# Kernel optimization log

Measured on AMD Instinct MI355X. Metric: run time of the kernel, lower is better.

The kernel has to match this reference:

```python
import jax, jax.numpy as jnp
import numpy as np


def setup_inputs() -> dict:
    key = jax.random.key(0)
    ks = jax.random.split(key, 7)
    B, T, D = 4, 4096, 128
    s = 0.02
    return {
        "input_data": jax.random.normal(ks[0], (B, T, D), dtype=jnp.float32),
        "Wq": jax.random.normal(ks[1], (D, D), dtype=jnp.float32) * s,
        "bq": jax.random.normal(ks[2], (D,), dtype=jnp.float32) * s,
        "Wk": jax.random.normal(ks[3], (D, D), dtype=jnp.float32) * s,
        "bk": jax.random.normal(ks[4], (D,), dtype=jnp.float32) * s,
        "Wv": jax.random.normal(ks[5], (D, D), dtype=jnp.float32) * s,
        "bv": jax.random.normal(ks[6], (D,), dtype=jnp.float32) * s,
    }


def reference(input_data, Wq, bq, Wk, bk, Wv, bv):
    D = input_data.shape[-1]
    scale = jnp.asarray(D, input_data.dtype) ** 0.5
    # torch Linear: x @ W.T + b
    q = input_data @ Wq.T + bq  # [B,T,D]
    k = input_data @ Wk.T + bk
    v = input_data @ Wv.T + bv
    energy = jnp.einsum("btd,bsd->bts", q, k) / scale  # [B,T,T]
    attn = jax.nn.softmax(energy, axis=-1)
    return jnp.einsum("bts,bsd->btd", attn, v)  # [B,T,D]
```

## Files before the change

kernel.cpp:

```cpp
#include <hip/hip_runtime.h>
#include <cstdint>

typedef _Float16 half4_t __attribute__((ext_vector_type(4)));
typedef _Float16 half8_t __attribute__((ext_vector_type(8)));
typedef float floatx4 __attribute__((ext_vector_type(4)));

#define T_SEQ 4096
#define D_HEAD 128
#define SCALE_LOG2 0.12751742526f

__device__ __forceinline__ void gload16(const void* src, void* dst_lds) {
    using gptr_t = const __attribute__((address_space(1))) unsigned int*;
    using lptr_t = __attribute__((address_space(3))) unsigned int*;
    __builtin_amdgcn_global_load_lds((gptr_t)(uintptr_t)src,
                                     (lptr_t)(unsigned int)(uintptr_t)dst_lds, 16, 0, 0);
}

__global__ __launch_bounds__(256) void proj_kernel(
    const float* __restrict__ x,
    const float* __restrict__ Wq, const float* __restrict__ bq,
    const float* __restrict__ Wk, const float* __restrict__ bk,
    const float* __restrict__ Wv, const float* __restrict__ bv,
    _Float16* __restrict__ qf, _Float16* __restrict__ kf, _Float16* __restrict__ vt)
{
    __shared__ __align__(16) _Float16 Ws[128 * 136];
    __shared__ __align__(16) _Float16 xs[64 * 136];

    const int t = threadIdx.x;
    const int mat = blockIdx.y;
    const float* W = (mat == 0) ? Wq : (mat == 1) ? Wk : Wv;
    const float* bias = (mat == 0) ? bq : (mat == 1) ? bk : bv;
    const float osc = (mat == 0) ? SCALE_LOG2 : 1.0f;
    const int r0 = blockIdx.x * 64;

    {
        const int o = t >> 1;
        const int i0 = (t & 1) * 64;
        for (int jj = 0; jj < 8; ++jj) {
            floatx4 w0 = *reinterpret_cast<const floatx4*>(W + o * 128 + i0 + jj * 8);
            floatx4 w1 = *reinterpret_cast<const floatx4*>(W + o * 128 + i0 + jj * 8 + 4);
            half8_t h;
            h[0]=(_Float16)w0[0]; h[1]=(_Float16)w0[1]; h[2]=(_Float16)w0[2]; h[3]=(_Float16)w0[3];
            h[4]=(_Float16)w1[0]; h[5]=(_Float16)w1[1]; h[6]=(_Float16)w1[2]; h[7]=(_Float16)w1[3];
            *reinterpret_cast<half8_t*>(&Ws[o * 136 + i0 + jj * 8]) = h;
        }
    }
    {
        const int row = t >> 2;
        const int c0 = (t & 3) * 32;
        for (int jj = 0; jj < 4; ++jj) {
            floatx4 w0 = *reinterpret_cast<const floatx4*>(x + (size_t)(r0 + row) * 128 + c0 + jj * 8);
            floatx4 w1 = *reinterpret_cast<const floatx4*>(x + (size_t)(r0 + row) * 128 + c0 + jj * 8 + 4);
            half8_t h;
            h[0]=(_Float16)w0[0]; h[1]=(_Float16)w0[1]; h[2]=(_Float16)w0[2]; h[3]=(_Float16)w0[3];
            h[4]=(_Float16)w1[0]; h[5]=(_Float16)w1[1]; h[6]=(_Float16)w1[2]; h[7]=(_Float16)w1[3];
            *reinterpret_cast<half8_t*>(&xs[row * 136 + c0 + jj * 8]) = h;
        }
    }
    __syncthreads();

    const int w = t >> 6;
    const int lane = t & 63;
    const int lo = lane & 15, hi = lane >> 4;

    floatx4 acc[8] = {};
    for (int dc = 0; dc < 4; ++dc) {
        half8_t a8 = *reinterpret_cast<const half8_t*>(&xs[(w * 16 + lo) * 136 + dc * 32 + hi * 8]);
        for (int ot = 0; ot < 8; ++ot) {
            half8_t b8 = *reinterpret_cast<const half8_t*>(&Ws[(ot * 16 + lo) * 136 + dc * 32 + hi * 8]);
            acc[ot] = __builtin_amdgcn_mfma_f32_16x16x32_f16(a8, b8, acc[ot], 0, 0, 0);
        }
    }
    __syncthreads();

    float bb[8];
    for (int ot = 0; ot < 8; ++ot) bb[ot] = bias[ot * 16 + lo];

    if (mat < 2) {
        _Float16* ol = xs;
        for (int ot = 0; ot < 8; ++ot)
            for (int r = 0; r < 4; ++r)
                ol[(w * 16 + hi * 4 + r) * 136 + ot * 16 + lo] = (_Float16)((acc[ot][r] + bb[ot]) * osc);
        __syncthreads();
        _Float16* dst = (mat == 0) ? qf : kf;
        for (int i = 0; i < 4; ++i) {
            int c = t + 256 * i;
            int row = c >> 4, p = c & 15;
            half8_t v = *reinterpret_cast<const half8_t*>(&ol[row * 136 + p * 8]);
            *reinterpret_cast<half8_t*>(dst + (size_t)(r0 + row) * 128 + p * 8) = v;
        }
    } else {
        _Float16* vl = Ws;
        for (int ot = 0; ot < 8; ++ot)
            for (int r = 0; r < 4; ++r)
                vl[(ot * 16 + lo) * 72 + w * 16 + hi * 4 + r] = (_Float16)(acc[ot][r] + bb[ot]);
        __syncthreads();
        const int b = r0 >> 12, tl0 = r0 & 4095;
        for (int i = 0; i < 4; ++i) {
            int c = t + 256 * i;
            int d = c >> 3, p = c & 7;
            half8_t v = *reinterpret_cast<const half8_t*>(&vl[d * 72 + p * 8]);
            *reinterpret_cast<half8_t*>(vt + ((size_t)(b * 128 + d)) * 4096 + tl0 + p * 8) = v;
        }
    }
}

__global__ __launch_bounds__(512, 2) void attn_kernel(
    const _Float16* __restrict__ qf, const _Float16* __restrict__ kf,
    const _Float16* __restrict__ vt, float* __restrict__ out)
{
    __shared__ __align__(16) char smem[131072];

    const int tid = threadIdx.x;
    const int w = tid >> 6, lane = tid & 63;
    const int lo = lane & 15, hi = lane >> 4;
    const int qsub = w & 1, split = w >> 1;

    const int bx = blockIdx.x;
    const int wg = (bx & 7) * 32 + (bx >> 3);
    const int b = wg >> 6;
    const int q0 = (wg & 63) * 64;

    const char* kbc = (const char*)(kf + (size_t)b * T_SEQ * 128);
    const char* vbc = (const char*)(vt + (size_t)b * 128 * T_SEQ);

    int koff[4], voff[4], kdst[4], vdst[4];
#pragma unroll
    for (int r = 0; r < 4; ++r) {
        int seg = w * 4 + r;
        int slot = lane & 15;
        int row = seg * 4 + (lane >> 4);
        koff[r] = row * 256 + ((slot ^ (row & 7)) << 4);
        kdst[r] = seg * 1024 + lane * 16;
        int d = row;
        voff[r] = d * (T_SEQ * 2) + ((slot ^ ((d & 7) << 1)) << 4);
        vdst[r] = 32768 + seg * 1024 + lane * 16;
    }

    half8_t qfrag[2][4];
#pragma unroll
    for (int qt = 0; qt < 2; ++qt) {
        const _Float16* qrow = qf + ((size_t)b * T_SEQ + q0 + qsub * 32 + qt * 16 + lo) * 128;
#pragma unroll
        for (int dc = 0; dc < 4; ++dc)
            qfrag[qt][dc] = *reinterpret_cast<const half8_t*>(qrow + dc * 32 + hi * 8);
    }

    floatx4 accO[2][8] = {};
    float m_run[2] = {-1e30f, -1e30f}, l_run[2] = {0.f, 0.f};

#pragma unroll
    for (int r = 0; r < 4; ++r) {
        gload16(kbc + koff[r], smem + kdst[r]);
        gload16(vbc + voff[r], smem + vdst[r]);
    }
    __syncthreads();

    for (int t0 = 0; t0 < T_SEQ; t0 += 128) {
        const int cur = (t0 >> 7) & 1;
        char* buf = smem + (cur << 16);

        if (t0 + 128 < T_SEQ) {
            char* nb = smem + ((cur ^ 1) << 16);
            const char* ks = kbc + (size_t)(t0 + 128) * 256;
            const char* vs = vbc + (size_t)(t0 + 128) * 2;
#pragma unroll
            for (int r = 0; r < 4; ++r) {
                gload16(ks + koff[r], nb + kdst[r]);
                gload16(vs + voff[r], nb + vdst[r]);
            }
        }

        floatx4 sac[2][2] = {};
#pragma unroll
        for (int s = 0; s < 2; ++s) {
            const char* kb0 = buf + (split * 32 + s * 16 + lo) * 256;
            const int rsw = lo & 7;
#pragma unroll
            for (int dc = 0; dc < 4; ++dc) {
                half8_t kf8 = *reinterpret_cast<const half8_t*>(kb0 + (((dc * 4 + hi) ^ rsw) << 4));
                sac[0][s] = __builtin_amdgcn_mfma_f32_16x16x32_f16(kf8, qfrag[0][dc], sac[0][s], 0, 0, 0);
                sac[1][s] = __builtin_amdgcn_mfma_f32_16x16x32_f16(kf8, qfrag[1][dc], sac[1][s], 0, 0, 0);
            }
        }

        float bm[2];
        bool ok = true;
#pragma unroll
        for (int qt = 0; qt < 2; ++qt) {
            float m0 = fmaxf(fmaxf(sac[qt][0][0], sac[qt][0][1]), fmaxf(sac[qt][0][2], sac[qt][0][3]));
            float m1 = fmaxf(fmaxf(sac[qt][1][0], sac[qt][1][1]), fmaxf(sac[qt][1][2], sac[qt][1][3]));
            float m = fmaxf(m0, m1);
            m = fmaxf(m, __shfl_xor(m, 16));
            m = fmaxf(m, __shfl_xor(m, 32));
            bm[qt] = m;
            ok = ok && (m <= m_run[qt] + 4.0f);
        }
        if (!__all(ok)) {
#pragma unroll
            for (int qt = 0; qt < 2; ++qt) {
                float m_new = fmaxf(m_run[qt], bm[qt]);
                float alpha = exp2f(m_run[qt] - m_new);
                l_run[qt] *= alpha;
#pragma unroll
                for (int dt = 0; dt < 8; ++dt) accO[qt][dt] *= alpha;
                m_run[qt] = m_new;
            }
        }
        half8_t pa[2];
#pragma unroll
        for (int qt = 0; qt < 2; ++qt) {
            float bs = 0.f;
            half8_t pp;
#pragma unroll
            for (int s = 0; s < 2; ++s)
#pragma unroll
                for (int r = 0; r < 4; ++r) {
                    float pv = exp2f(sac[qt][s][r] - m_run[qt]);
                    bs += pv;
                    pp[s * 4 + r] = (_Float16)pv;
                }
            bs += __shfl_xor(bs, 16);
            bs += __shfl_xor(bs, 32);
            l_run[qt] += bs;
            pa[qt] = pp;
        }

        const char* vbuf = buf + 32768;
#pragma unroll
        for (int dt = 0; dt < 8; ++dt) {
            int row = dt * 16 + lo;
            const char* vr = vbuf + row * 256;
            int sw = (row & 7) << 1;
            int c0 = split * 4 + (hi >> 1);
            half4_t va = *reinterpret_cast<const half4_t*>(vr + (((c0) ^ sw) << 4) + ((hi & 1) << 3));
            half4_t vb4 = *reinterpret_cast<const half4_t*>(vr + (((c0 + 2) ^ sw) << 4) + ((hi & 1) << 3));
            half8_t vfr;
            vfr[0]=va[0]; vfr[1]=va[1]; vfr[2]=va[2]; vfr[3]=va[3];
            vfr[4]=vb4[0]; vfr[5]=vb4[1]; vfr[6]=vb4[2]; vfr[7]=vb4[3];
            accO[0][dt] = __builtin_amdgcn_mfma_f32_16x16x32_f16(vfr, pa[0], accO[0][dt], 0, 0, 0);
            accO[1][dt] = __builtin_amdgcn_mfma_f32_16x16x32_f16(vfr, pa[1], accO[1][dt], 0, 0, 0);
        }
        __syncthreads();
    }

    float* red_m = reinterpret_cast<float*>(smem + 65536);
    float* red_l = reinterpret_cast<float*>(smem + 65536 + 1024);
    int row64[2]; float fac[2];
#pragma unroll
    for (int qt = 0; qt < 2; ++qt) row64[qt] = qsub * 32 + qt * 16 + lo;
    if (hi == 0) {
#pragma unroll
        for (int qt = 0; qt < 2; ++qt) {
            red_m[split * 64 + row64[qt]] = m_run[qt];
            red_l[split * 64 + row64[qt]] = l_run[qt];
        }
    }
    __syncthreads();
#pragma unroll
    for (int qt = 0; qt < 2; ++qt) {
        float M = -1e30f;
#pragma unroll
        for (int s = 0; s < 4; ++s) M = fmaxf(M, red_m[s * 64 + row64[qt]]);
        float L = 0.f;
#pragma unroll
        for (int s = 0; s < 4; ++s) L += red_l[s * 64 + row64[qt]] * exp2f(red_m[s * 64 + row64[qt]] - M);
        fac[qt] = exp2f(m_run[qt] - M) / L;
    }
    float* out_lds = reinterpret_cast<float*>(smem);
    for (int s = 0; s < 4; ++s) {
        if (split == s) {
#pragma unroll
            for (int qt = 0; qt < 2; ++qt)
#pragma unroll
                for (int dt = 0; dt < 8; ++dt)
#pragma unroll
                    for (int r = 0; r < 4; ++r) {
                        int d = dt * 16 + hi * 4 + r;
                        float v = accO[qt][dt][r] * fac[qt];
                        float* p = &out_lds[row64[qt] * 132 + d];
                        if (s == 0) *p = v; else *p += v;
                    }
        }
        __syncthreads();
    }
    {
        int row = tid >> 3, d0 = (tid & 7) * 16;
        float* op = out + ((size_t)b * T_SEQ + q0 + row) * 128 + d0;
#pragma unroll
        for (int j = 0; j < 4; ++j) {
            float4 v;
            v.x = out_lds[row * 132 + d0 + j * 4 + 0];
            v.y = out_lds[row * 132 + d0 + j * 4 + 1];
            v.z = out_lds[row * 132 + d0 + j * 4 + 2];
            v.w = out_lds[row * 132 + d0 + j * 4 + 3];
            *reinterpret_cast<float4*>(op + j * 4) = v;
        }
    }
}

extern "C" void kernel_launch(void* const* d_in, const int* in_sizes, int n_in,
                              void* d_out, int out_size, void* d_ws, size_t ws_size,
                              hipStream_t stream)
{
    (void)in_sizes; (void)n_in; (void)out_size; (void)ws_size;
    const float* x  = (const float*)d_in[0];
    const float* Wq = (const float*)d_in[1];
    const float* bq = (const float*)d_in[2];
    const float* Wk = (const float*)d_in[3];
    const float* bk = (const float*)d_in[4];
    const float* Wv = (const float*)d_in[5];
    const float* bv = (const float*)d_in[6];
    float* out = (float*)d_out;

    _Float16* qf = (_Float16*)d_ws;
    _Float16* kf = qf + (size_t)4 * T_SEQ * D_HEAD;
    _Float16* vt = kf + (size_t)4 * T_SEQ * D_HEAD;

    proj_kernel<<<dim3(256, 3), 256, 0, stream>>>(x, Wq, bq, Wk, bk, Wv, bv, qf, kf, vt);
    attn_kernel<<<dim3(256), 512, 0, stream>>>(qf, kf, vt, out);
}
```

Baseline: 94.97 us.

## Use 16 waves per attention block, one 16-row query tile per wave

The attention kernel moves from 512 to 1024 threads per block. Each wave now owns a single 16-row query tile instead of two, which halves per-wave accumulators and softmax state and doubles the waves per CU available to hide latency. Each block-wide K/V tile load is split over twice as many threads. The V tile swizzle changes to a plain row-based XOR, with load and read updated to match. s_setprio is raised around the MFMA sections. The cost is that each K and V fragment read from LDS now feeds only one MFMA instead of two, so LDS read traffic per FLOP doubles.

```diff
diff --git a/kernel.cpp b/kernel.cpp
--- a/kernel.cpp
+++ b/kernel.cpp
@@ -105,7 +105,7 @@
     }
 }
 
-__global__ __launch_bounds__(512, 2) void attn_kernel(
+__global__ __launch_bounds__(1024) void attn_kernel(
     const _Float16* __restrict__ qf, const _Float16* __restrict__ kf,
     const _Float16* __restrict__ vt, float* __restrict__ out)
 {
@@ -114,7 +114,7 @@
     const int tid = threadIdx.x;
     const int w = tid >> 6, lane = tid & 63;
     const int lo = lane & 15, hi = lane >> 4;
-    const int qsub = w & 1, split = w >> 1;
+    const int qsub = w & 3, split = w >> 2;
 
     const int bx = blockIdx.x;
     const int wg = (bx & 7) * 32 + (bx >> 3);
@@ -124,33 +124,31 @@
     const char* kbc = (const char*)(kf + (size_t)b * T_SEQ * 128);
     const char* vbc = (const char*)(vt + (size_t)b * 128 * T_SEQ);
 
-    int koff[4], voff[4], kdst[4], vdst[4];
-#pragma unroll
-    for (int r = 0; r < 4; ++r) {
-        int seg = w * 4 + r;
+    int koff[2], voff[2], kdst[2], vdst[2];
+#pragma unroll
+    for (int r = 0; r < 2; ++r) {
+        int seg = w * 2 + r;
         int slot = lane & 15;
         int row = seg * 4 + (lane >> 4);
         koff[r] = row * 256 + ((slot ^ (row & 7)) << 4);
         kdst[r] = seg * 1024 + lane * 16;
-        int d = row;
-        voff[r] = d * (T_SEQ * 2) + ((slot ^ ((d & 7) << 1)) << 4);
+        voff[r] = row * (T_SEQ * 2) + ((slot ^ (row & 7)) << 4);
         vdst[r] = 32768 + seg * 1024 + lane * 16;
     }
 
-    half8_t qfrag[2][4];
-#pragma unroll
-    for (int qt = 0; qt < 2; ++qt) {
-        const _Float16* qrow = qf + ((size_t)b * T_SEQ + q0 + qsub * 32 + qt * 16 + lo) * 128;
+    half8_t qfrag[4];
+    {
+        const _Float16* qrow = qf + ((size_t)b * T_SEQ + q0 + qsub * 16 + lo) * 128;
 #pragma unroll
         for (int dc = 0; dc < 4; ++dc)
-            qfrag[qt][dc] = *reinterpret_cast<const half8_t*>(qrow + dc * 32 + hi * 8);
-    }
-
-    floatx4 accO[2][8] = {};
-    float m_run[2] = {-1e30f, -1e30f}, l_run[2] = {0.f, 0.f};
-
-#pragma unroll
-    for (int r = 0; r < 4; ++r) {
+            qfrag[dc] = *reinterpret_cast<const half8_t*>(qrow + dc * 32 + hi * 8);
+    }
+
+    floatx4 accO[8] = {};
+    float m_run = -1e30f, l_run = 0.f;
+
+#pragma unroll
+    for (int r = 0; r < 2; ++r) {
         gload16(kbc + koff[r], smem + kdst[r]);
         gload16(vbc + voff[r], smem + vdst[r]);
     }
@@ -165,13 +163,14 @@
             const char* ks = kbc + (size_t)(t0 + 128) * 256;
             const char* vs = vbc + (size_t)(t0 + 128) * 2;
 #pragma unroll
-            for (int r = 0; r < 4; ++r) {
+            for (int r = 0; r < 2; ++r) {
                 gload16(ks + koff[r], nb + kdst[r]);
                 gload16(vs + voff[r], nb + vdst[r]);
             }
         }
 
-        floatx4 sac[2][2] = {};
+        floatx4 sac[2] = {};
+        __builtin_amdgcn_s_setprio(1);
 #pragma unroll
         for (int s = 0; s < 2; ++s) {
             const char* kb0 = buf + (split * 32 + s * 16 + lo) * 256;
@@ -179,116 +178,93 @@
 #pragma unroll
             for (int dc = 0; dc < 4; ++dc) {
                 half8_t kf8 = *reinterpret_cast<const half8_t*>(kb0 + (((dc * 4 + hi) ^ rsw) << 4));
-                sac[0][s] = __builtin_amdgcn_mfma_f32_16x16x32_f16(kf8, qfrag[0][dc], sac[0][s], 0, 0, 0);
-                sac[1][s] = __builtin_amdgcn_mfma_f32_16x16x32_f16(kf8, qfrag[1][dc], sac[1][s], 0, 0, 0);
+                sac[s] = __builtin_amdgcn_mfma_f32_16x16x32_f16(kf8, qfrag[dc], sac[s], 0, 0, 0);
             }
         }
-
-        float bm[2];
-        bool ok = true;
-#pragma unroll
-        for (int qt = 0; qt < 2; ++qt) {
-            float m0 = fmaxf(fmaxf(sac[qt][0][0], sac[qt][0][1]), fmaxf(sac[qt][0][2], sac[qt][0][3]));
-            float m1 = fmaxf(fmaxf(sac[qt][1][0], sac[qt][1][1]), fmaxf(sac[qt][1][2], sac[qt][1][3]));
-            float m = fmaxf(m0, m1);
-            m = fmaxf(m, __shfl_xor(m, 16));
-            m = fmaxf(m, __shfl_xor(m, 32));
-            bm[qt] = m;
-            ok = ok && (m <= m_run[qt] + 4.0f);
-        }
+        __builtin_amdgcn_s_setprio(0);
+
+        float m = fmaxf(fmaxf(fmaxf(sac[0][0], sac[0][1]), fmaxf(sac[0][2], sac[0][3])),
+                        fmaxf(fmaxf(sac[1][0], sac[1][1]), fmaxf(sac[1][2], sac[1][3])));
+        m = fmaxf(m, __shfl_xor(m, 16));
+        m = fmaxf(m, __shfl_xor(m, 32));
+        bool ok = (m <= m_run + 4.0f);
         if (!__all(ok)) {
-#pragma unroll
-            for (int qt = 0; qt < 2; ++qt) {
-                float m_new = fmaxf(m_run[qt], bm[qt]);
-                float alpha = exp2f(m_run[qt] - m_new);
-                l_run[qt] *= alpha;
-#pragma unroll
-                for (int dt = 0; dt < 8; ++dt) accO[qt][dt] *= alpha;
-                m_run[qt] = m_new;
+            float m_new = fmaxf(m_run, m);
+            float alpha = exp2f(m_run - m_new);
+            l_run *= alpha;
+#pragma unroll
+            for (int dt = 0; dt < 8; ++dt) accO[dt] *= alpha;
+            m_run = m_new;
+        }
+        half8_t pa;
+        float bs = 0.f;
+#pragma unroll
+        for (int s = 0; s < 2; ++s)
+#pragma unroll
+            for (int r = 0; r < 4; ++r) {
+                float pv = exp2f(sac[s][r] - m_run);
+                bs += pv;
+                pa[s * 4 + r] = (_Float16)pv;
             }
-        }
-        half8_t pa[2];
-#pragma unroll
-        for (int qt = 0; qt < 2; ++qt) {
-            float bs = 0.f;
-            half8_t pp;
-#pragma unroll
-            for (int s = 0; s < 2; ++s)
-#pragma unroll
-                for (int r = 0; r < 4; ++r) {
-                    float pv = exp2f(sac[qt][s][r] - m_run[qt]);
-                    bs += pv;
-                    pp[s * 4 + r] = (_Float16)pv;
-                }
-            bs += __shfl_xor(bs, 16);
-            bs += __shfl_xor(bs, 32);
-            l_run[qt] += bs;
-            pa[qt] = pp;
-        }
+        bs += __shfl_xor(bs, 16);
+        bs += __shfl_xor(bs, 32);
+        l_run += bs;
 
         const char* vbuf = buf + 32768;
+        __builtin_amdgcn_s_setprio(1);
 #pragma unroll
         for (int dt = 0; dt < 8; ++dt) {
             int row = dt * 16 + lo;
             const char* vr = vbuf + row * 256;
-            int sw = (row & 7) << 1;
+            int sw = lo & 7;
             int c0 = split * 4 + (hi >> 1);
-            half4_t va = *reinterpret_cast<const half4_t*>(vr + (((c0) ^ sw) << 4) + ((hi & 1) << 3));
+            half4_t va  = *reinterpret_cast<const half4_t*>(vr + ((c0 ^ sw) << 4) + ((hi & 1) << 3));
             half4_t vb4 = *reinterpret_cast<const half4_t*>(vr + (((c0 + 2) ^ sw) << 4) + ((hi & 1) << 3));
             half8_t vfr;
             vfr[0]=va[0]; vfr[1]=va[1]; vfr[2]=va[2]; vfr[3]=va[3];
             vfr[4]=vb4[0]; vfr[5]=vb4[1]; vfr[6]=vb4[2]; vfr[7]=vb4[3];
-            accO[0][dt] = __builtin_amdgcn_mfma_f32_16x16x32_f16(vfr, pa[0], accO[0][dt], 0, 0, 0);
-            accO[1][dt] = __builtin_amdgcn_mfma_f32_16x16x32_f16(vfr, pa[1], accO[1][dt], 0, 0, 0);
-        }
-        __syncthreads();
-    }
-
-    float* red_m = reinterpret_cast<float*>(smem + 65536);
-    float* red_l = reinterpret_cast<float*>(smem + 65536 + 1024);
-    int row64[2]; float fac[2];
-#pragma unroll
-    for (int qt = 0; qt < 2; ++qt) row64[qt] = qsub * 32 + qt * 16 + lo;
+            accO[dt] = __builtin_amdgcn_mfma_f32_16x16x32_f16(vfr, pa, accO[dt], 0, 0, 0);
+        }
+        __builtin_amdgcn_s_setprio(0);
+        __syncthreads();
+    }
+
+    float* red_m = reinterpret_cast<float*>(smem + 40960);
+    float* red_l = reinterpret_cast<float*>(smem + 43008);
+    const int row16 = qsub * 16 + lo;
     if (hi == 0) {
-#pragma unroll
-        for (int qt = 0; qt < 2; ++qt) {
-            red_m[split * 64 + row64[qt]] = m_run[qt];
-            red_l[split * 64 + row64[qt]] = l_run[qt];
-        }
-    }
-    __syncthreads();
-#pragma unroll
-    for (int qt = 0; qt < 2; ++qt) {
-        float M = -1e30f;
-#pragma unroll
-        for (int s = 0; s < 4; ++s) M = fmaxf(M, red_m[s * 64 + row64[qt]]);
-        float L = 0.f;
-#pragma unroll
-        for (int s = 0; s < 4; ++s) L += red_l[s * 64 + row64[qt]] * exp2f(red_m[s * 64 + row64[qt]] - M);
-        fac[qt] = exp2f(m_run[qt] - M) / L;
-    }
+        red_m[split * 64 + row16] = m_run;
+        red_l[split * 64 + row16] = l_run;
+    }
+    __syncthreads();
+    float M = -1e30f;
+#pragma unroll
+    for (int s = 0; s < 4; ++s) M = fmaxf(M, red_m[s * 64 + row16]);
+    float L = 0.f;
+#pragma unroll
+    for (int s = 0; s < 4; ++s) L += red_l[s * 64 + row16] * exp2f(red_m[s * 64 + row16] - M);
+    const float fac = exp2f(m_run - M) / L;
+
     float* out_lds = reinterpret_cast<float*>(smem);
     for (int s = 0; s < 4; ++s) {
         if (split == s) {
 #pragma unroll
-            for (int qt = 0; qt < 2; ++qt)
-#pragma unroll
-                for (int dt = 0; dt < 8; ++dt)
-#pragma unroll
-                    for (int r = 0; r < 4; ++r) {
-                        int d = dt * 16 + hi * 4 + r;
-                        float v = accO[qt][dt][r] * fac[qt];
-                        float* p = &out_lds[row64[qt] * 132 + d];
-                        if (s == 0) *p = v; else *p += v;
-                    }
-        }
-        __syncthreads();
-    }
-    {
-        int row = tid >> 3, d0 = (tid & 7) * 16;
+            for (int dt = 0; dt < 8; ++dt)
+#pragma unroll
+                for (int r = 0; r < 4; ++r) {
+                    int d = dt * 16 + hi * 4 + r;
+                    float v = accO[dt][r] * fac;
+                    float* p = &out_lds[row16 * 132 + d];
+                    if (s == 0) *p = v; else *p += v;
+                }
+        }
+        __syncthreads();
+    }
+    {
+        int row = tid >> 4, d0 = (tid & 15) * 8;
         float* op = out + ((size_t)b * T_SEQ + q0 + row) * 128 + d0;
 #pragma unroll
-        for (int j = 0; j < 4; ++j) {
+        for (int j = 0; j < 2; ++j) {
             float4 v;
             v.x = out_lds[row * 132 + d0 + j * 4 + 0];
             v.y = out_lds[row * 132 + d0 + j * 4 + 1];
@@ -318,5 +294,5 @@
     _Float16* vt = kf + (size_t)4 * T_SEQ * D_HEAD;
 
     proj_kernel<<<dim3(256, 3), 256, 0, stream>>>(x, Wq, bq, Wk, bk, Wv, bv, qf, kf, vt);
-    attn_kernel<<<dim3(256), 512, 0, stream>>>(qf, kf, vt, out);
-}
+    attn_kernel<<<dim3(256), 1024, 0, stream>>>(qf, kf, vt, out);
+}
```

Result: faster. 92.05 us (-3.1%).

## Stage V tiles through registers with repacked LDS layout, unroll loop, set MFMA priority

Applied to the files above, without the earlier changes.

The V tile prefetch now goes through registers and is written to LDS only after the PV MFMAs. The LDS layout is permuted so each PV operand becomes a single 16-byte read instead of two 8-byte reads plus a shuffle. The main loop is manually unrolled by two with constant buffer offsets and precomputed LDS addresses, s_setprio raises wave priority around the MFMA blocks, and P is converted with packed round-to-zero fp16. Launch bounds drop to one block per CU, which allows more registers per thread at the cost of less occupancy, and the reduction scratch moves to a different LDS offset.

```diff
diff --git a/kernel.cpp b/kernel.cpp
--- a/kernel.cpp
+++ b/kernel.cpp
@@ -1,6 +1,7 @@
 #include <hip/hip_runtime.h>
 #include <cstdint>
 
+typedef _Float16 half2_t __attribute__((ext_vector_type(2)));
 typedef _Float16 half4_t __attribute__((ext_vector_type(4)));
 typedef _Float16 half8_t __attribute__((ext_vector_type(8)));
 typedef float floatx4 __attribute__((ext_vector_type(4)));
@@ -105,7 +106,7 @@
     }
 }
 
-__global__ __launch_bounds__(512, 2) void attn_kernel(
+__global__ __launch_bounds__(512, 1) void attn_kernel(
     const _Float16* __restrict__ qf, const _Float16* __restrict__ kf,
     const _Float16* __restrict__ vt, float* __restrict__ out)
 {
@@ -114,7 +115,7 @@
     const int tid = threadIdx.x;
     const int w = tid >> 6, lane = tid & 63;
     const int lo = lane & 15, hi = lane >> 4;
-    const int qsub = w & 1, split = w >> 1;
+    const int qt2 = w & 1, split = w >> 1;
 
     const int bx = blockIdx.x;
     const int wg = (bx & 7) * 32 + (bx >> 3);
@@ -124,7 +125,7 @@
     const char* kbc = (const char*)(kf + (size_t)b * T_SEQ * 128);
     const char* vbc = (const char*)(vt + (size_t)b * 128 * T_SEQ);
 
-    int koff[4], voff[4], kdst[4], vdst[4];
+    int koff[4], kdst[4];
 #pragma unroll
     for (int r = 0; r < 4; ++r) {
         int seg = w * 4 + r;
@@ -132,15 +133,35 @@
         int row = seg * 4 + (lane >> 4);
         koff[r] = row * 256 + ((slot ^ (row & 7)) << 4);
         kdst[r] = seg * 1024 + lane * 16;
-        int d = row;
-        voff[r] = d * (T_SEQ * 2) + ((slot ^ ((d & 7) << 1)) << 4);
-        vdst[r] = 32768 + seg * 1024 + lane * 16;
-    }
+    }
+
+    const int vc = tid & 15;
+    const int vua = ((vc >> 2) << 2) + ((vc & 1) << 1);
+    const int voffb = (vc & 2) << 2;
+    int vgo[4], vwa[4], vwb[4];
+#pragma unroll
+    for (int i = 0; i < 4; ++i) {
+        int d = (tid >> 4) + 32 * i;
+        vgo[i] = d * (T_SEQ * 2) + vc * 16;
+        vwa[i] = 32768 + d * 256 + (((vua)     ^ (d & 7)) << 4) + voffb;
+        vwb[i] = 32768 + d * 256 + (((vua + 1) ^ (d & 7)) << 4) + voffb;
+    }
+
+    int kro[2][4];
+#pragma unroll
+    for (int s = 0; s < 2; ++s)
+#pragma unroll
+        for (int dc = 0; dc < 4; ++dc)
+            kro[s][dc] = (split * 32 + s * 16 + lo) * 256 + ((((dc * 4 + hi)) ^ (lo & 7)) << 4);
+    int vro[8];
+#pragma unroll
+    for (int dt = 0; dt < 8; ++dt)
+        vro[dt] = 32768 + (dt * 16 + lo) * 256 + (((split * 4 + hi) ^ (lo & 7)) << 4);
 
     half8_t qfrag[2][4];
 #pragma unroll
     for (int qt = 0; qt < 2; ++qt) {
-        const _Float16* qrow = qf + ((size_t)b * T_SEQ + q0 + qsub * 32 + qt * 16 + lo) * 128;
+        const _Float16* qrow = qf + ((size_t)b * T_SEQ + q0 + qt2 * 32 + qt * 16 + lo) * 128;
 #pragma unroll
         for (int dc = 0; dc < 4; ++dc)
             qfrag[qt][dc] = *reinterpret_cast<const half8_t*>(qrow + dc * 32 + hi * 8);
@@ -150,105 +171,117 @@
     float m_run[2] = {-1e30f, -1e30f}, l_run[2] = {0.f, 0.f};
 
 #pragma unroll
-    for (int r = 0; r < 4; ++r) {
-        gload16(kbc + koff[r], smem + kdst[r]);
-        gload16(vbc + voff[r], smem + vdst[r]);
+    for (int r = 0; r < 4; ++r) gload16(kbc + koff[r], smem + kdst[r]);
+    {
+        uint4 vreg[4];
+#pragma unroll
+        for (int i = 0; i < 4; ++i) vreg[i] = *reinterpret_cast<const uint4*>(vbc + vgo[i]);
+#pragma unroll
+        for (int i = 0; i < 4; ++i) {
+            *reinterpret_cast<uint2*>(smem + vwa[i]) = make_uint2(vreg[i].x, vreg[i].y);
+            *reinterpret_cast<uint2*>(smem + vwb[i]) = make_uint2(vreg[i].z, vreg[i].w);
+        }
     }
     __syncthreads();
 
-    for (int t0 = 0; t0 < T_SEQ; t0 += 128) {
-        const int cur = (t0 >> 7) & 1;
-        char* buf = smem + (cur << 16);
-
-        if (t0 + 128 < T_SEQ) {
-            char* nb = smem + ((cur ^ 1) << 16);
-            const char* ks = kbc + (size_t)(t0 + 128) * 256;
-            const char* vs = vbc + (size_t)(t0 + 128) * 2;
-#pragma unroll
-            for (int r = 0; r < 4; ++r) {
-                gload16(ks + koff[r], nb + kdst[r]);
-                gload16(vs + voff[r], nb + vdst[r]);
-            }
-        }
-
-        floatx4 sac[2][2] = {};
-#pragma unroll
-        for (int s = 0; s < 2; ++s) {
-            const char* kb0 = buf + (split * 32 + s * 16 + lo) * 256;
-            const int rsw = lo & 7;
-#pragma unroll
-            for (int dc = 0; dc < 4; ++dc) {
-                half8_t kf8 = *reinterpret_cast<const half8_t*>(kb0 + (((dc * 4 + hi) ^ rsw) << 4));
-                sac[0][s] = __builtin_amdgcn_mfma_f32_16x16x32_f16(kf8, qfrag[0][dc], sac[0][s], 0, 0, 0);
-                sac[1][s] = __builtin_amdgcn_mfma_f32_16x16x32_f16(kf8, qfrag[1][dc], sac[1][s], 0, 0, 0);
-            }
-        }
-
-        float bm[2];
-        bool ok = true;
-#pragma unroll
-        for (int qt = 0; qt < 2; ++qt) {
-            float m0 = fmaxf(fmaxf(sac[qt][0][0], sac[qt][0][1]), fmaxf(sac[qt][0][2], sac[qt][0][3]));
-            float m1 = fmaxf(fmaxf(sac[qt][1][0], sac[qt][1][1]), fmaxf(sac[qt][1][2], sac[qt][1][3]));
-            float m = fmaxf(m0, m1);
-            m = fmaxf(m, __shfl_xor(m, 16));
-            m = fmaxf(m, __shfl_xor(m, 32));
-            bm[qt] = m;
-            ok = ok && (m <= m_run[qt] + 4.0f);
-        }
-        if (!__all(ok)) {
-#pragma unroll
-            for (int qt = 0; qt < 2; ++qt) {
-                float m_new = fmaxf(m_run[qt], bm[qt]);
-                float alpha = exp2f(m_run[qt] - m_new);
-                l_run[qt] *= alpha;
-#pragma unroll
-                for (int dt = 0; dt < 8; ++dt) accO[qt][dt] *= alpha;
-                m_run[qt] = m_new;
-            }
-        }
-        half8_t pa[2];
-#pragma unroll
-        for (int qt = 0; qt < 2; ++qt) {
-            float bs = 0.f;
-            half8_t pp;
-#pragma unroll
-            for (int s = 0; s < 2; ++s)
-#pragma unroll
-                for (int r = 0; r < 4; ++r) {
-                    float pv = exp2f(sac[qt][s][r] - m_run[qt]);
-                    bs += pv;
-                    pp[s * 4 + r] = (_Float16)pv;
-                }
-            bs += __shfl_xor(bs, 16);
-            bs += __shfl_xor(bs, 32);
-            l_run[qt] += bs;
-            pa[qt] = pp;
-        }
-
-        const char* vbuf = buf + 32768;
-#pragma unroll
-        for (int dt = 0; dt < 8; ++dt) {
-            int row = dt * 16 + lo;
-            const char* vr = vbuf + row * 256;
-            int sw = (row & 7) << 1;
-            int c0 = split * 4 + (hi >> 1);
-            half4_t va = *reinterpret_cast<const half4_t*>(vr + (((c0) ^ sw) << 4) + ((hi & 1) << 3));
-            half4_t vb4 = *reinterpret_cast<const half4_t*>(vr + (((c0 + 2) ^ sw) << 4) + ((hi & 1) << 3));
-            half8_t vfr;
-            vfr[0]=va[0]; vfr[1]=va[1]; vfr[2]=va[2]; vfr[3]=va[3];
-            vfr[4]=vb4[0]; vfr[5]=vb4[1]; vfr[6]=vb4[2]; vfr[7]=vb4[3];
-            accO[0][dt] = __builtin_amdgcn_mfma_f32_16x16x32_f16(vfr, pa[0], accO[0][dt], 0, 0, 0);
-            accO[1][dt] = __builtin_amdgcn_mfma_f32_16x16x32_f16(vfr, pa[1], accO[1][dt], 0, 0, 0);
-        }
-        __syncthreads();
-    }
-
-    float* red_m = reinterpret_cast<float*>(smem + 65536);
-    float* red_l = reinterpret_cast<float*>(smem + 65536 + 1024);
+#define TILE(T0, CUR, NXT, PF) do {                                                    \
+    uint4 vreg[4];                                                                     \
+    if (PF) {                                                                          \
+        const char* vs = vbc + (size_t)((T0) + 128) * 2;                               \
+        _Pragma("unroll")                                                              \
+        for (int i = 0; i < 4; ++i)                                                    \
+            vreg[i] = *reinterpret_cast<const uint4*>(vs + vgo[i]);                    \
+        const char* ks = kbc + (size_t)((T0) + 128) * 256;                             \
+        _Pragma("unroll")                                                              \
+        for (int r = 0; r < 4; ++r) gload16(ks + koff[r], smem + (NXT) + kdst[r]);     \
+    }                                                                                  \
+    const char* bufc = smem + (CUR);                                                   \
+    floatx4 sac[2][2] = {};                                                            \
+    __builtin_amdgcn_s_setprio(1);                                                     \
+    _Pragma("unroll")                                                                  \
+    for (int s = 0; s < 2; ++s) {                                                      \
+        _Pragma("unroll")                                                              \
+        for (int dc = 0; dc < 4; ++dc) {                                               \
+            half8_t kf8 = *reinterpret_cast<const half8_t*>(bufc + kro[s][dc]);        \
+            sac[0][s] = __builtin_amdgcn_mfma_f32_16x16x32_f16(kf8, qfrag[0][dc], sac[0][s], 0, 0, 0); \
+            sac[1][s] = __builtin_amdgcn_mfma_f32_16x16x32_f16(kf8, qfrag[1][dc], sac[1][s], 0, 0, 0); \
+        }                                                                              \
+    }                                                                                  \
+    __builtin_amdgcn_s_setprio(0);                                                     \
+    float bm[2];                                                                       \
+    bool ok = true;                                                                    \
+    _Pragma("unroll")                                                                  \
+    for (int qt = 0; qt < 2; ++qt) {                                                   \
+        float m0 = fmaxf(fmaxf(sac[qt][0][0], sac[qt][0][1]), fmaxf(sac[qt][0][2], sac[qt][0][3])); \
+        float m1 = fmaxf(fmaxf(sac[qt][1][0], sac[qt][1][1]), fmaxf(sac[qt][1][2], sac[qt][1][3])); \
+        float m = fmaxf(m0, m1);                                                       \
+        m = fmaxf(m, __shfl_xor(m, 16));                                               \
+        m = fmaxf(m, __shfl_xor(m, 32));                                               \
+        bm[qt] = m;                                                                    \
+        ok = ok && (m <= m_run[qt] + 4.0f);                                            \
+    }                                                                                  \
+    if (!__all(ok)) {                                                                  \
+        _Pragma("unroll")                                                              \
+        for (int qt = 0; qt < 2; ++qt) {                                               \
+            float m_new = fmaxf(m_run[qt], bm[qt]);                                    \
+            float alpha = exp2f(m_run[qt] - m_new);                                    \
+            l_run[qt] *= alpha;                                                        \
+            _Pragma("unroll")                                                          \
+            for (int dt = 0; dt < 8; ++dt) accO[qt][dt] *= alpha;                      \
+            m_run[qt] = m_new;                                                         \
+        }                                                                              \
+    }                                                                                  \
+    half8_t pa[2];                                                                     \
+    _Pragma("unroll")                                                                  \
+    for (int qt = 0; qt < 2; ++qt) {                                                   \
+        float pv[8];                                                                   \
+        float bs = 0.f;                                                                \
+        _Pragma("unroll")                                                              \
+        for (int j = 0; j < 8; ++j) {                                                  \
+            int s = j >> 2, r = j & 3;                                                 \
+            pv[j] = exp2f(sac[qt][s][r] - m_run[qt]);                                  \
+            bs += pv[j];                                                               \
+        }                                                                              \
+        bs += __shfl_xor(bs, 16);                                                      \
+        bs += __shfl_xor(bs, 32);                                                      \
+        l_run[qt] += bs;                                                               \
+        _Pragma("unroll")                                                              \
+        for (int j2 = 0; j2 < 4; ++j2) {                                               \
+            half2_t h2 = __builtin_bit_cast(half2_t,                                   \
+                __builtin_amdgcn_cvt_pkrtz(pv[j2 * 2], pv[j2 * 2 + 1]));               \
+            pa[qt][j2 * 2] = h2[0];                                                    \
+            pa[qt][j2 * 2 + 1] = h2[1];                                                \
+        }                                                                              \
+    }                                                                                  \
+    __builtin_amdgcn_s_setprio(1);                                                     \
+    _Pragma("unroll")                                                                  \
+    for (int dt = 0; dt < 8; ++dt) {                                                   \
+        half8_t vfr = *reinterpret_cast<const half8_t*>(bufc + vro[dt]);               \
+        accO[0][dt] = __builtin_amdgcn_mfma_f32_16x16x32_f16(vfr, pa[0], accO[0][dt], 0, 0, 0); \
+        accO[1][dt] = __builtin_amdgcn_mfma_f32_16x16x32_f16(vfr, pa[1], accO[1][dt], 0, 0, 0); \
+    }                                                                                  \
+    __builtin_amdgcn_s_setprio(0);                                                     \
+    if (PF) {                                                                          \
+        _Pragma("unroll")                                                              \
+        for (int i = 0; i < 4; ++i) {                                                  \
+            *reinterpret_cast<uint2*>(smem + (NXT) + vwa[i]) = make_uint2(vreg[i].x, vreg[i].y); \
+            *reinterpret_cast<uint2*>(smem + (NXT) + vwb[i]) = make_uint2(vreg[i].z, vreg[i].w); \
+        }                                                                              \
+    }                                                                                  \
+    __syncthreads();                                                                   \
+} while (0)
+
+    for (int t0 = 0; t0 < T_SEQ; t0 += 256) {
+        TILE(t0, 0, 65536, true);
+        TILE(t0 + 128, 65536, 0, (t0 + 256 < T_SEQ));
+    }
+#undef TILE
+
+    float* red_m = reinterpret_cast<float*>(smem + 40960);
+    float* red_l = reinterpret_cast<float*>(smem + 43008);
     int row64[2]; float fac[2];
 #pragma unroll
-    for (int qt = 0; qt < 2; ++qt) row64[qt] = qsub * 32 + qt * 16 + lo;
+    for (int qt = 0; qt < 2; ++qt) row64[qt] = qt2 * 32 + qt * 16 + lo;
     if (hi == 0) {
 #pragma unroll
         for (int qt = 0; qt < 2; ++qt) {
```

After: 85.29 us. 1.11x faster.
